# Performance work log

Measured on AMD Instinct MI355X. Metric: run time of the kernel, lower is better.

## Reference

```python
import jax, jax.numpy as jnp
import numpy as np


def setup_inputs() -> dict:
    key = jax.random.key(0)
    ks = jax.random.split(key, 8)
    B, H, W, C = 4, 64, 64, 256
    d = C // 8  # 32
    s = 0.02
    return {
        "x": jax.random.normal(ks[0], (B, H, W, C), dtype=jnp.float32),
        "Wq": jax.random.normal(ks[1], (C, d), dtype=jnp.float32) * s,
        "bq": jnp.zeros((d,), dtype=jnp.float32),
        "Wk": jax.random.normal(ks[2], (C, d), dtype=jnp.float32) * s,
        "bk": jnp.zeros((d,), dtype=jnp.float32),
        "Wv": jax.random.normal(ks[3], (C, C), dtype=jnp.float32) * s,
        "bv": jnp.zeros((C,), dtype=jnp.float32),
        "gamma": jnp.zeros((1,), dtype=jnp.float32),
    }


def reference(x, Wq, bq, Wk, bk, Wv, bv, gamma):
    B, H, W, C = x.shape
    N = H * W
    xf = x.reshape(B, N, C)                       # 1x1 conv == per-pixel matmul
    q = xf @ Wq + bq                              # [B, N, C//8]
    k = xf @ Wk + bk                              # [B, N, C//8]
    v = xf @ Wv + bv                              # [B, N, C]
    attn = jax.nn.softmax(jnp.einsum('bnd,bmd->bnm', q, k), axis=-1)  # [B, N, N]
    out = jnp.einsum('bnm,bmc->bnc', attn, v).reshape(B, H, W, C)
    return gamma * out + x
```

## Files before the change

kernel.cpp:

```cpp
#include <hip/hip_runtime.h>
#include <hip/hip_bf16.h>

typedef __bf16 bf16;
typedef __bf16 bf16x8 __attribute__((ext_vector_type(8)));
typedef __bf16 bf16x4 __attribute__((ext_vector_type(4)));
typedef float f32x4 __attribute__((ext_vector_type(4)));

static __device__ __forceinline__ f32x4 mfma16(bf16x8 a, bf16x8 b, f32x4 c) {
  return __builtin_amdgcn_mfma_f32_16x16x32_bf16(a, b, c, 0, 0, 0);
}

static __device__ __forceinline__ void wg_barrier() {
  asm volatile("s_waitcnt lgkmcnt(0)" ::: "memory");
  __builtin_amdgcn_s_barrier();
  asm volatile("" ::: "memory");
}

static __device__ __forceinline__ bf16x8 cvt8(const float* p) {
  f32x4 a0 = *(const f32x4*)p;
  f32x4 a1 = *(const f32x4*)(p + 4);
  bf16x8 r;
#pragma unroll
  for (int j = 0; j < 4; ++j) { r[j] = (bf16)a0[j]; r[4 + j] = (bf16)a1[j]; }
  return r;
}

__global__ void prep_wt(const float* __restrict__ Wq, const float* __restrict__ Wk,
                        const float* __restrict__ Wv, bf16* __restrict__ Wf) {
  int k = blockIdx.x;
  int c = threadIdx.x;
  float v;
  if (c < 32)       v = Wq[k * 32 + c];
  else if (c < 64)  v = Wk[k * 32 + (c - 32)];
  else              v = Wv[k * 256 + (c - 64)];
  int t5 = c >> 6, ct = (c >> 4) & 3, lwc = c & 15;
  int kc = k >> 5, qq = (k >> 3) & 3, ke = k & 7;
  Wf[((((t5 * 8 + kc) * 4 + ct) * 64) + qq * 16 + lwc) * 8 + ke] = (bf16)v;
}

__global__ __launch_bounds__(256) void qkv_gemm(
    const float* __restrict__ x, const bf16* __restrict__ Wf,
    const float* __restrict__ bq, const float* __restrict__ bk,
    const float* __restrict__ bv,
    bf16* __restrict__ Qd, bf16* __restrict__ Kd, bf16* __restrict__ Vt) {
  __shared__ __align__(16) bf16 tile[64 * 72];
  int tid = threadIdx.x;
  int lane = tid & 63, w = tid >> 6;
  int lw = lane & 15, qq = lane >> 4;
  int r0 = blockIdx.x * 64;
  int bb = r0 >> 12, n0 = r0 & 4095;

  const float* arow = x + (size_t)(r0 + 16 * w + lw) * 256;
  bf16x8 a[8];
#pragma unroll
  for (int kc = 0; kc < 8; ++kc) a[kc] = cvt8(arow + kc * 32 + qq * 8);

  for (int c0 = 0; c0 < 320; c0 += 64) {
    int t5 = c0 >> 6;
    f32x4 acc[4] = {};
#pragma unroll
    for (int kc = 0; kc < 8; ++kc)
#pragma unroll
      for (int t = 0; t < 4; ++t) {
        bf16x8 b = *(const bf16x8*)(Wf + ((size_t)(((t5 * 8 + kc) * 4 + t) * 64) + lane) * 8);
        acc[t] = mfma16(a[kc], b, acc[t]);
      }
    if (c0 == 0) {
#pragma unroll
      for (int t = 0; t < 4; ++t) {
        int c = 16 * t + lw;
        float bias = (c < 32) ? bq[c] : bk[c - 32];
#pragma unroll
        for (int i = 0; i < 4; ++i) {
          int n = n0 + 16 * w + 4 * qq + i;
          bf16 hv = (bf16)(acc[t][i] + bias);
          if (c < 32) Qd[((size_t)(bb << 12) + n) * 32 + c] = hv;
          else        Kd[((size_t)(bb << 12) + n) * 32 + (c - 32)] = hv;
        }
      }
    } else {
#pragma unroll
      for (int t = 0; t < 4; ++t) {
        int cl = 16 * t + lw;
        float bias = bv[c0 - 64 + cl];
#pragma unroll
        for (int i = 0; i < 4; ++i)
          tile[cl * 72 + 16 * w + 4 * qq + i] = (bf16)(acc[t][i] + bias);
      }
      __syncthreads();
      int nl = tid & 63;
#pragma unroll
      for (int it = 0; it < 16; ++it) {
        int cl = 4 * it + w;
        Vt[((size_t)bb * 256 + (c0 - 64) + cl) * 4096 + n0 + nl] = tile[cl * 72 + nl];
      }
      __syncthreads();
    }
  }
}

__global__ __launch_bounds__(512, 2) void flash_attn(
    const bf16* __restrict__ Qd, const bf16* __restrict__ Kd,
    const bf16* __restrict__ Vt, const float* __restrict__ x,
    const float* __restrict__ gamma, float* __restrict__ out) {
  __shared__ __align__(16) bf16 Pl[2][64 * 72];
  __shared__ float lsum[4][64];

  int tid = threadIdx.x;
  int lane = tid & 63, w = tid >> 6;
  int lw = lane & 15, qq = lane >> 4;
  int bb = blockIdx.y;
  int r0 = blockIdx.x * 64;

  const bf16* Qb = Qd + ((size_t)bb << 12) * 32;
  const bf16* Kb = Kd + ((size_t)bb << 12) * 32;
  const bf16* Vb = Vt + (size_t)bb * 256 * 4096;

  if (w < 4) {
    int kvs = 16 * w;
    bf16x8 qfp[4];
#pragma unroll
    for (int qt = 0; qt < 4; ++qt)
      qfp[qt] = *(const bf16x8*)(Qb + (size_t)(r0 + 16 * qt + lw) * 32 + qq * 8);
    float l_part[4] = {};
    bf16x8 kA, kB;

    kA = *(const bf16x8*)(Kb + (size_t)(kvs + lw) * 32 + qq * 8);
#pragma unroll
    for (int qt = 0; qt < 4; ++qt) {
      f32x4 z = {};
      f32x4 s = mfma16(kA, qfp[qt], z);
      bf16x4 pk;
#pragma unroll
      for (int i = 0; i < 4; ++i) { float p = __expf(s[i]); l_part[qt] += p; pk[i] = (bf16)p; }
      *(bf16x4*)&Pl[0][(16 * qt + lw) * 72 + kvs + 4 * qq] = pk;
    }
    kB = *(const bf16x8*)(Kb + (size_t)(64 + kvs + lw) * 32 + qq * 8);
    wg_barrier();

#define PROD_PH(J, PN, KC, KN)                                                 \
    {                                                                          \
      const int j = (J);                                                       \
      if (j < 63) {                                                            \
        _Pragma("unroll") for (int qt = 0; qt < 4; ++qt) {                     \
          f32x4 z = {};                                                        \
          f32x4 s = mfma16(KC, qfp[qt], z);                                    \
          bf16x4 pk;                                                           \
          _Pragma("unroll") for (int i = 0; i < 4; ++i) {                      \
            float p = __expf(s[i]); l_part[qt] += p; pk[i] = (bf16)p;          \
          }                                                                    \
          *(bf16x4*)&Pl[PN][(16 * qt + lw) * 72 + kvs + 4 * qq] = pk;          \
        }                                                                      \
        int n2 = ((j + 2) & 63) * 64;                                          \
        KN = *(const bf16x8*)(Kb + (size_t)(n2 + kvs + lw) * 32 + qq * 8);     \
      }                                                                        \
      wg_barrier();                                                            \
    }

    for (int jj = 0; jj < 32; ++jj) {
      PROD_PH(2 * jj,     1, kB, kA)
      PROD_PH(2 * jj + 1, 0, kA, kB)
    }
#undef PROD_PH

#pragma unroll
    for (int qt = 0; qt < 4; ++qt) {
      float v = l_part[qt];
      v += __shfl_xor(v, 16);
      v += __shfl_xor(v, 32);
      if (qq == 0) lsum[w][16 * qt + lw] = v;
    }
    __syncthreads();
  } else {
    int chb = 64 * (w - 4);
    f32x4 o[4][4] = {};
    bf16x8 vA[8], vB[8];
#pragma unroll
    for (int t = 0; t < 4; ++t)
#pragma unroll
      for (int kc = 0; kc < 2; ++kc)
        vA[t * 2 + kc] = *(const bf16x8*)(Vb + (size_t)(chb + 16 * t + lw) * 4096 + kc * 32 + qq * 8);
    wg_barrier();

#define CONS_PH(J, PC, VC, VN)                                                 \
    {                                                                          \
      const int j = (J);                                                       \
      int n1 = ((j + 1) & 63) * 64;                                            \
      bf16x8 af[4][2];                                                         \
      _Pragma("unroll") for (int m = 0; m < 4; ++m)                            \
        _Pragma("unroll") for (int kc = 0; kc < 2; ++kc)                       \
          af[m][kc] = *(const bf16x8*)&Pl[PC][(16 * m + lw) * 72 + kc * 32 + qq * 8]; \
      _Pragma("unroll") for (int t = 0; t < 4; ++t)                            \
        _Pragma("unroll") for (int kc = 0; kc < 2; ++kc)                       \
          VN[t * 2 + kc] = *(const bf16x8*)(Vb + (size_t)(chb + 16 * t + lw) * 4096 + n1 + kc * 32 + qq * 8); \
      _Pragma("unroll") for (int kc = 0; kc < 2; ++kc)                         \
        _Pragma("unroll") for (int t = 0; t < 4; ++t)                          \
          _Pragma("unroll") for (int m = 0; m < 4; ++m)                        \
            o[m][t] = mfma16(af[m][kc], VC[t * 2 + kc], o[m][t]);              \
      wg_barrier();                                                            \
    }

    for (int jj = 0; jj < 32; ++jj) {
      CONS_PH(2 * jj,     0, vA, vB)
      CONS_PH(2 * jj + 1, 1, vB, vA)
    }
#undef CONS_PH

    __syncthreads();

    float g = gamma[0];
#pragma unroll
    for (int m = 0; m < 4; ++m) {
      f32x4 l0 = *(const f32x4*)&lsum[0][16 * m + 4 * qq];
      f32x4 l1 = *(const f32x4*)&lsum[1][16 * m + 4 * qq];
      f32x4 l2 = *(const f32x4*)&lsum[2][16 * m + 4 * qq];
      f32x4 l3 = *(const f32x4*)&lsum[3][16 * m + 4 * qq];
#pragma unroll
      for (int i = 0; i < 4; ++i) {
        float rinv = 1.f / (l0[i] + l1[i] + l2[i] + l3[i]);
        int row = r0 + 16 * m + 4 * qq + i;
        size_t base = (((size_t)bb << 12) + row) * 256 + chb;
#pragma unroll
        for (int t = 0; t < 4; ++t)
          out[base + 16 * t + lw] = g * (o[m][t][i] * rinv) + x[base + 16 * t + lw];
      }
    }
  }
}

extern "C" void kernel_launch(void* const* d_in, const int* in_sizes, int n_in,
                              void* d_out, int out_size, void* d_ws, size_t ws_size,
                              hipStream_t stream) {
  const float* x     = (const float*)d_in[0];
  const float* Wq    = (const float*)d_in[1];
  const float* bq    = (const float*)d_in[2];
  const float* Wk    = (const float*)d_in[3];
  const float* bk    = (const float*)d_in[4];
  const float* Wv    = (const float*)d_in[5];
  const float* bv    = (const float*)d_in[6];
  const float* gamma = (const float*)d_in[7];
  float* out = (float*)d_out;

  const size_t WT_E = 320 * 256;
  const size_t QK_E = (size_t)4096 * 32;
  const size_t VT_E = (size_t)256 * 4096;
  size_t full_bytes = (WT_E + 4 * 2 * QK_E + 4 * VT_E) * sizeof(bf16);

  bf16* Wf = (bf16*)d_ws;
  prep_wt<<<dim3(256), dim3(320), 0, stream>>>(Wq, Wk, Wv, Wf);

  if (ws_size >= full_bytes) {
    bf16* Qd = Wf + WT_E;
    bf16* Kd = Qd + 4 * QK_E;
    bf16* Vt = Kd + 4 * QK_E;
    qkv_gemm<<<dim3(256), dim3(256), 0, stream>>>(x, Wf, bq, bk, bv, Qd, Kd, Vt);
    flash_attn<<<dim3(64, 4), dim3(512), 0, stream>>>(Qd, Kd, Vt, x, gamma, out);
  } else {
    bf16* Qd = Wf + WT_E;
    bf16* Kd = Qd + QK_E;
    bf16* Vt = Kd + QK_E;
    for (int b = 0; b < 4; ++b) {
      const float* xb = x + (size_t)b * 4096 * 256;
      float* outb = out + (size_t)b * 4096 * 256;
      qkv_gemm<<<dim3(64), dim3(256), 0, stream>>>(xb, Wf, bq, bk, bv, Qd, Kd, Vt);
      flash_attn<<<dim3(64, 1), dim3(512), 0, stream>>>(Qd, Kd, Vt, xb, gamma, outb);
    }
  }
}
```

Baseline: 159.3 us.

## Process two KV tiles per barrier phase with four-slot P buffer

The producer/consumer warp-specialized attention loop now handles two 64-key tiles per barrier step instead of one. The shared P buffer grows to four slots, and producers compute two P tiles per phase. Consumers run two tiles of PV MFMAs per phase, reloading each tile's V registers right after use. This halves the number of workgroup barriers and gives each phase more independent work to overlap. In exchange it uses more LDS, which could reduce occupancy at two blocks per CU, and keeps two V register sets live.

```diff
diff --git a/kernel.cpp b/kernel.cpp
--- a/kernel.cpp
+++ b/kernel.cpp
@@ -103,7 +103,7 @@
     const bf16* __restrict__ Qd, const bf16* __restrict__ Kd,
     const bf16* __restrict__ Vt, const float* __restrict__ x,
     const float* __restrict__ gamma, float* __restrict__ out) {
-  __shared__ __align__(16) bf16 Pl[2][64 * 72];
+  __shared__ __align__(16) bf16 Pl[4][64 * 72];
   __shared__ float lsum[4][64];
 
   int tid = threadIdx.x;
@@ -123,45 +123,45 @@
     for (int qt = 0; qt < 4; ++qt)
       qfp[qt] = *(const bf16x8*)(Qb + (size_t)(r0 + 16 * qt + lw) * 32 + qq * 8);
     float l_part[4] = {};
-    bf16x8 kA, kB;
-
-    kA = *(const bf16x8*)(Kb + (size_t)(kvs + lw) * 32 + qq * 8);
-#pragma unroll
-    for (int qt = 0; qt < 4; ++qt) {
-      f32x4 z = {};
-      f32x4 s = mfma16(kA, qfp[qt], z);
-      bf16x4 pk;
-#pragma unroll
-      for (int i = 0; i < 4; ++i) { float p = __expf(s[i]); l_part[qt] += p; pk[i] = (bf16)p; }
-      *(bf16x4*)&Pl[0][(16 * qt + lw) * 72 + kvs + 4 * qq] = pk;
-    }
-    kB = *(const bf16x8*)(Kb + (size_t)(64 + kvs + lw) * 32 + qq * 8);
+    bf16x8 kbA, kbB;
+
+#define PROD_TILE(PS, KREG)                                                    \
+    _Pragma("unroll") for (int qt = 0; qt < 4; ++qt) {                         \
+      f32x4 z = {};                                                            \
+      f32x4 s = mfma16(KREG, qfp[qt], z);                                      \
+      bf16x4 pk;                                                               \
+      _Pragma("unroll") for (int i = 0; i < 4; ++i) {                          \
+        float p = __expf(s[i]); l_part[qt] += p; pk[i] = (bf16)p;              \
+      }                                                                        \
+      *(bf16x4*)&Pl[PS][(16 * qt + lw) * 72 + kvs + 4 * qq] = pk;              \
+    }
+
+    kbA = *(const bf16x8*)(Kb + (size_t)(kvs + lw) * 32 + qq * 8);
+    kbB = *(const bf16x8*)(Kb + (size_t)(64 + kvs + lw) * 32 + qq * 8);
+    PROD_TILE(0, kbA)
+    PROD_TILE(1, kbB)
+    kbA = *(const bf16x8*)(Kb + (size_t)(128 + kvs + lw) * 32 + qq * 8);
+    kbB = *(const bf16x8*)(Kb + (size_t)(192 + kvs + lw) * 32 + qq * 8);
     wg_barrier();
 
-#define PROD_PH(J, PN, KC, KN)                                                 \
+#define PROD_SP(SS, WS0, WS1)                                                  \
     {                                                                          \
-      const int j = (J);                                                       \
-      if (j < 63) {                                                            \
-        _Pragma("unroll") for (int qt = 0; qt < 4; ++qt) {                     \
-          f32x4 z = {};                                                        \
-          f32x4 s = mfma16(KC, qfp[qt], z);                                    \
-          bf16x4 pk;                                                           \
-          _Pragma("unroll") for (int i = 0; i < 4; ++i) {                      \
-            float p = __expf(s[i]); l_part[qt] += p; pk[i] = (bf16)p;          \
-          }                                                                    \
-          *(bf16x4*)&Pl[PN][(16 * qt + lw) * 72 + kvs + 4 * qq] = pk;          \
-        }                                                                      \
-        int n2 = ((j + 2) & 63) * 64;                                          \
-        KN = *(const bf16x8*)(Kb + (size_t)(n2 + kvs + lw) * 32 + qq * 8);     \
+      const int c0 = 2 * (SS) + 2;                                             \
+      if (c0 < 64) {                                                           \
+        PROD_TILE(WS0, kbA)                                                    \
+        kbA = *(const bf16x8*)(Kb + (size_t)((((c0 + 2) & 63) * 64) + kvs + lw) * 32 + qq * 8); \
+        PROD_TILE(WS1, kbB)                                                    \
+        kbB = *(const bf16x8*)(Kb + (size_t)((((c0 + 3) & 63) * 64) + kvs + lw) * 32 + qq * 8); \
       }                                                                        \
       wg_barrier();                                                            \
     }
 
-    for (int jj = 0; jj < 32; ++jj) {
-      PROD_PH(2 * jj,     1, kB, kA)
-      PROD_PH(2 * jj + 1, 0, kA, kB)
-    }
-#undef PROD_PH
+    for (int jj = 0; jj < 16; ++jj) {
+      PROD_SP(2 * jj,     2, 3)
+      PROD_SP(2 * jj + 1, 0, 1)
+    }
+#undef PROD_SP
+#undef PROD_TILE
 
 #pragma unroll
     for (int qt = 0; qt < 4; ++qt) {
@@ -175,36 +175,46 @@
     int chb = 64 * (w - 4);
     f32x4 o[4][4] = {};
     bf16x8 vA[8], vB[8];
-#pragma unroll
-    for (int t = 0; t < 4; ++t)
-#pragma unroll
-      for (int kc = 0; kc < 2; ++kc)
-        vA[t * 2 + kc] = *(const bf16x8*)(Vb + (size_t)(chb + 16 * t + lw) * 4096 + kc * 32 + qq * 8);
-    wg_barrier();
-
-#define CONS_PH(J, PC, VC, VN)                                                 \
+
+#define CONS_TILE(PS, VREGS, NV)                                               \
     {                                                                          \
-      const int j = (J);                                                       \
-      int n1 = ((j + 1) & 63) * 64;                                            \
       bf16x8 af[4][2];                                                         \
       _Pragma("unroll") for (int m = 0; m < 4; ++m)                            \
         _Pragma("unroll") for (int kc = 0; kc < 2; ++kc)                       \
-          af[m][kc] = *(const bf16x8*)&Pl[PC][(16 * m + lw) * 72 + kc * 32 + qq * 8]; \
-      _Pragma("unroll") for (int t = 0; t < 4; ++t)                            \
-        _Pragma("unroll") for (int kc = 0; kc < 2; ++kc)                       \
-          VN[t * 2 + kc] = *(const bf16x8*)(Vb + (size_t)(chb + 16 * t + lw) * 4096 + n1 + kc * 32 + qq * 8); \
+          af[m][kc] = *(const bf16x8*)&Pl[PS][(16 * m + lw) * 72 + kc * 32 + qq * 8]; \
       _Pragma("unroll") for (int kc = 0; kc < 2; ++kc)                         \
         _Pragma("unroll") for (int t = 0; t < 4; ++t)                          \
           _Pragma("unroll") for (int m = 0; m < 4; ++m)                        \
-            o[m][t] = mfma16(af[m][kc], VC[t * 2 + kc], o[m][t]);              \
+            o[m][t] = mfma16(af[m][kc], VREGS[t * 2 + kc], o[m][t]);           \
+      _Pragma("unroll") for (int t = 0; t < 4; ++t)                            \
+        _Pragma("unroll") for (int kc = 0; kc < 2; ++kc)                       \
+          VREGS[t * 2 + kc] = *(const bf16x8*)(Vb + (size_t)(chb + 16 * t + lw) * 4096 + (NV) + kc * 32 + qq * 8); \
+    }
+
+#pragma unroll
+    for (int t = 0; t < 4; ++t)
+#pragma unroll
+      for (int kc = 0; kc < 2; ++kc) {
+        vA[t * 2 + kc] = *(const bf16x8*)(Vb + (size_t)(chb + 16 * t + lw) * 4096 + kc * 32 + qq * 8);
+        vB[t * 2 + kc] = *(const bf16x8*)(Vb + (size_t)(chb + 16 * t + lw) * 4096 + 64 + kc * 32 + qq * 8);
+      }
+    wg_barrier();
+
+#define CONS_SP(SS, RS0, RS1)                                                  \
+    {                                                                          \
+      const int c0 = 2 * (SS);                                                 \
+      int nv0 = ((c0 + 2) & 63) * 64, nv1 = ((c0 + 3) & 63) * 64;              \
+      CONS_TILE(RS0, vA, nv0)                                                  \
+      CONS_TILE(RS1, vB, nv1)                                                  \
       wg_barrier();                                                            \
     }
 
-    for (int jj = 0; jj < 32; ++jj) {
-      CONS_PH(2 * jj,     0, vA, vB)
-      CONS_PH(2 * jj + 1, 1, vB, vA)
-    }
-#undef CONS_PH
+    for (int jj = 0; jj < 16; ++jj) {
+      CONS_SP(2 * jj,     0, 1)
+      CONS_SP(2 * jj + 1, 2, 3)
+    }
+#undef CONS_SP
+#undef CONS_TILE
 
     __syncthreads();
 
```

Result: no change. 160.4 us (+0.7%).
